# Performance work log

Measured on AMD Instinct MI355X. Metric: run time of the kernel, lower is better.

## Reference

```python
import jax, jax.numpy as jnp
import numpy as np

B, S, D = 8, 2048, 512  # batch, seq_len, lstm_hidden_dim


def setup_inputs() -> dict:
    key = jax.random.key(0)
    kq, kk, kv = jax.random.split(key, 3)
    return {
        "query": jax.random.normal(kq, (B, S, D), dtype=jnp.float32),
        "key": jax.random.normal(kk, (B, S, D), dtype=jnp.float32),
        "value": jax.random.normal(kv, (B, S, D), dtype=jnp.float32),
    }


def reference(query, key, value):
    hidden_dim = query.shape[-1]
    scale = 1.0 / jnp.sqrt(jnp.asarray(hidden_dim, dtype=jnp.float32))
    # scores: [B, S, S]
    scores = jnp.einsum("bqd,bkd->bqk", query, key) * scale
    attention_weights = jax.nn.softmax(scores, axis=-1)
    context = jnp.einsum("bqk,bkd->bqd", attention_weights, value)
    return (context, attention_weights)
```

## Files before the change

kernel.cpp:

```cpp
#include <hip/hip_runtime.h>


constexpr int BATCH = 8;
constexpr int SEQ = 2048;
constexpr int DIM = 512;
constexpr size_t QK_ELEMS = (size_t)BATCH * SEQ * DIM;

typedef __attribute__((ext_vector_type(8))) short bh8;
typedef __attribute__((ext_vector_type(4))) float f4acc;

__device__ __forceinline__ short f2bf(float f) {
  union { float f; unsigned u; } v;
  v.f = f;
  unsigned r = (v.u + 0x7FFFu + ((v.u >> 16) & 1u)) >> 16;
  return (short)r;
}

__device__ __forceinline__ void glds16(const unsigned short* g,
                                       unsigned short* l) {
  __builtin_amdgcn_global_load_lds(
      (const __attribute__((address_space(1))) unsigned int*)g,
      (__attribute__((address_space(3))) unsigned int*)l, 16, 0, 0);
}

__global__ __launch_bounds__(256) void convert_qk_kernel(
    const float* __restrict__ Q, const float* __restrict__ K,
    unsigned short* __restrict__ Qbf, unsigned short* __restrict__ Kbf) {
  const size_t i = ((size_t)blockIdx.x * 256 + threadIdx.x) * 8;
  const float sc = blockIdx.y ? 1.0f : 0.044194173824159216f;
  const float* src = blockIdx.y ? K : Q;
  unsigned short* dst = blockIdx.y ? Kbf : Qbf;
  float4 a = *(const float4*)(src + i);
  float4 b = *(const float4*)(src + i + 4);
  bh8 o;
  o[0] = f2bf(a.x * sc); o[1] = f2bf(a.y * sc);
  o[2] = f2bf(a.z * sc); o[3] = f2bf(a.w * sc);
  o[4] = f2bf(b.x * sc); o[5] = f2bf(b.y * sc);
  o[6] = f2bf(b.z * sc); o[7] = f2bf(b.w * sc);
  *(bh8*)(dst + i) = o;
}

__global__ __launch_bounds__(256) void transpose_v_kernel(
    const float* __restrict__ V, unsigned short* __restrict__ Vt) {
  __shared__ float tile[32][33];
  const int s0 = blockIdx.x * 32, d0 = blockIdx.y * 32, b = blockIdx.z;
  const float* Vb = V + (size_t)b * SEQ * DIM;
  unsigned short* Vtb = Vt + (size_t)b * DIM * SEQ;
  const int tx = threadIdx.x & 31, ty = threadIdx.x >> 5;
  for (int r = 0; r < 32; r += 8)
    tile[ty + r][tx] = Vb[(size_t)(s0 + ty + r) * DIM + (d0 + tx)];
  __syncthreads();
  for (int r = 0; r < 32; r += 8)
    Vtb[(size_t)(d0 + ty + r) * SEQ + (s0 + tx)] =
        (unsigned short)f2bf(tile[tx][ty + r]);
}

template <int KDIM, int NSTRIDE>
__device__ __forceinline__ void gemm_nt_body(
    const unsigned short* __restrict__ Arows,
    const unsigned short* __restrict__ Brows,
    float* __restrict__ Cout,
    unsigned short* As, unsigned short* Bs) {
  const int tid = threadIdx.x, lane = tid & 63, wave = tid >> 6;
  const int wm = (wave & 1) * 64, wn = (wave >> 1) * 64;
  const int srow = wave * 32 + (lane >> 2);
  const int scol = (lane & 3) * 8;
  const unsigned short* Ag = Arows + (size_t)srow * KDIM + scol;
  const unsigned short* Bg = Brows + (size_t)srow * KDIM + scol;
  unsigned short* Al = As + srow * 32 + scol;
  unsigned short* Bl = Bs + srow * 32 + scol;
  f4acc acc[4][4] = {};
  const int fr = lane & 15, fk = (lane >> 4) * 8;
  for (int k0 = 0; k0 < KDIM; k0 += 32) {
    glds16(Ag + k0, Al);
    glds16(Ag + k0 + (size_t)16 * KDIM, Al + 16 * 32);
    glds16(Bg + k0, Bl);
    glds16(Bg + k0 + (size_t)16 * KDIM, Bl + 16 * 32);
    __syncthreads();
    bh8 af[4], bf[4];
    for (int i = 0; i < 4; ++i) af[i] = *(const bh8*)(As + (wm + i * 16 + fr) * 32 + fk);
    for (int i = 0; i < 4; ++i) bf[i] = *(const bh8*)(Bs + (wn + i * 16 + fr) * 32 + fk);
    for (int mi = 0; mi < 4; ++mi)
      for (int ni = 0; ni < 4; ++ni)
        acc[mi][ni] = __builtin_amdgcn_mfma_f32_16x16x32_bf16(
            af[mi], bf[ni], acc[mi][ni], 0, 0, 0);
    __syncthreads();
  }
  const int cc = lane & 15, rr = (lane >> 4) * 4;
  for (int mi = 0; mi < 4; ++mi)
    for (int ni = 0; ni < 4; ++ni)
      for (int r = 0; r < 4; ++r)
        Cout[(size_t)(wm + mi * 16 + rr + r) * NSTRIDE + (wn + ni * 16 + cc)] =
            acc[mi][ni][r];
}

__global__ __launch_bounds__(256) void scores_kernel(
    const unsigned short* __restrict__ Qbf, const unsigned short* __restrict__ Kbf,
    float* __restrict__ W) {
  __shared__ unsigned short As[128 * 32];
  __shared__ unsigned short Bs[128 * 32];
  const int bm = blockIdx.x, bn = blockIdx.y, b = blockIdx.z;
  gemm_nt_body<DIM, SEQ>(
      Qbf + ((size_t)b * SEQ + bm * 128) * DIM,
      Kbf + ((size_t)b * SEQ + bn * 128) * DIM,
      W + (size_t)b * SEQ * SEQ + (size_t)(bm * 128) * SEQ + bn * 128, As, Bs);
}

__global__ __launch_bounds__(256) void context_kernel(
    const unsigned short* __restrict__ Wbf, const unsigned short* __restrict__ Vt,
    float* __restrict__ C) {
  __shared__ unsigned short As[128 * 32];
  __shared__ unsigned short Bs[128 * 32];
  const int bm = blockIdx.x, bn = blockIdx.y, b = blockIdx.z;
  gemm_nt_body<SEQ, DIM>(
      Wbf + ((size_t)b * SEQ + bm * 128) * SEQ,
      Vt + ((size_t)b * DIM + bn * 128) * SEQ,
      C + (size_t)b * SEQ * DIM + (size_t)(bm * 128) * DIM + bn * 128, As, Bs);
}

__global__ __launch_bounds__(256) void softmax_kernel(
    float* __restrict__ W, unsigned short* __restrict__ Wbf) {
  float* Wr = W + (size_t)blockIdx.x * SEQ;
  unsigned short* Wbr = Wbf + (size_t)blockIdx.x * SEQ;
  const int tid = threadIdx.x, lane = tid & 63, wave = tid >> 6;
  float4 a = ((const float4*)Wr)[tid];
  float4 c = ((const float4*)Wr)[tid + 256];
  float m = fmaxf(fmaxf(fmaxf(a.x, a.y), fmaxf(a.z, a.w)),
                  fmaxf(fmaxf(c.x, c.y), fmaxf(c.z, c.w)));
  for (int off = 32; off > 0; off >>= 1) m = fmaxf(m, __shfl_xor(m, off));
  __shared__ float redm[4];
  if (lane == 0) redm[wave] = m;
  __syncthreads();
  m = fmaxf(fmaxf(redm[0], redm[1]), fmaxf(redm[2], redm[3]));
  a.x = __expf(a.x - m); a.y = __expf(a.y - m);
  a.z = __expf(a.z - m); a.w = __expf(a.w - m);
  c.x = __expf(c.x - m); c.y = __expf(c.y - m);
  c.z = __expf(c.z - m); c.w = __expf(c.w - m);
  float s = (a.x + a.y + a.z + a.w) + (c.x + c.y + c.z + c.w);
  for (int off = 32; off > 0; off >>= 1) s += __shfl_xor(s, off);
  __shared__ float reds[4];
  if (lane == 0) reds[wave] = s;
  __syncthreads();
  s = reds[0] + reds[1] + reds[2] + reds[3];
  const float inv = 1.0f / s;
  a.x *= inv; a.y *= inv; a.z *= inv; a.w *= inv;
  c.x *= inv; c.y *= inv; c.z *= inv; c.w *= inv;
  ((float4*)Wr)[tid] = a;
  ((float4*)Wr)[tid + 256] = c;
  short4 ba = {f2bf(a.x), f2bf(a.y), f2bf(a.z), f2bf(a.w)};
  short4 bc = {f2bf(c.x), f2bf(c.y), f2bf(c.z), f2bf(c.w)};
  ((short4*)Wbr)[tid] = ba;
  ((short4*)Wbr)[tid + 256] = bc;
}

extern "C" void kernel_launch(void* const* d_in, const int* in_sizes, int n_in,
                              void* d_out, int out_size, void* d_ws,
                              size_t ws_size, hipStream_t stream) {
  const float* Q = (const float*)d_in[0];
  const float* K = (const float*)d_in[1];
  const float* V = (const float*)d_in[2];
  float* C = (float*)d_out;
  float* W = (float*)d_out + QK_ELEMS;
  unsigned short* Qbf = (unsigned short*)d_ws;
  unsigned short* Kbf = Qbf + QK_ELEMS;
  unsigned short* Vt  = Kbf + QK_ELEMS;
  unsigned short* Wbf = Vt + QK_ELEMS;

  convert_qk_kernel<<<dim3((unsigned)(QK_ELEMS / 8 / 256), 2), 256, 0, stream>>>(
      Q, K, Qbf, Kbf);
  transpose_v_kernel<<<dim3(SEQ / 32, DIM / 32, BATCH), 256, 0, stream>>>(V, Vt);
  scores_kernel<<<dim3(SEQ / 128, SEQ / 128, BATCH), 256, 0, stream>>>(Qbf, Kbf, W);
  softmax_kernel<<<dim3(BATCH * SEQ), 256, 0, stream>>>(W, Wbf);
  context_kernel<<<dim3(SEQ / 128, DIM / 128, BATCH), 256, 0, stream>>>(Wbf, Vt, C);
}
```

Baseline: 385.6 us.

## Store scores as bf16 via LDS staging and widen GEMM k-step to 64

The scores GEMM now writes bf16 scores into a separate workspace buffer, staged through LDS for coalesced 16-byte stores, instead of fp32 straight into the output. Softmax reads that bf16 buffer, cutting the fp32 score write and read traffic. The GEMM loop loads two 32-wide K slices per barrier pair, halving the number of syncs. Rounding scores to bf16 before softmax adds error to the attention weights, and the new buffer needs more workspace.

```diff
diff --git a/kernel.cpp b/kernel.cpp
--- a/kernel.cpp
+++ b/kernel.cpp
@@ -5,8 +5,10 @@
 constexpr int SEQ = 2048;
 constexpr int DIM = 512;
 constexpr size_t QK_ELEMS = (size_t)BATCH * SEQ * DIM;
+constexpr size_t SS_ELEMS = (size_t)BATCH * SEQ * SEQ;
 
 typedef __attribute__((ext_vector_type(8))) short bh8;
+typedef __attribute__((ext_vector_type(8))) unsigned short u16x8;
 typedef __attribute__((ext_vector_type(4))) float f4acc;
 
 __device__ __forceinline__ short f2bf(float f) {
@@ -14,6 +16,12 @@
   v.f = f;
   unsigned r = (v.u + 0x7FFFu + ((v.u >> 16) & 1u)) >> 16;
   return (short)r;
+}
+
+__device__ __forceinline__ float bf2f(unsigned short h) {
+  union { unsigned u; float f; } v;
+  v.u = (unsigned)h << 16;
+  return v.f;
 }
 
 __device__ __forceinline__ void glds16(const unsigned short* g,
@@ -55,102 +63,130 @@
         (unsigned short)f2bf(tile[tx][ty + r]);
 }
 
-template <int KDIM, int NSTRIDE>
-__device__ __forceinline__ void gemm_nt_body(
-    const unsigned short* __restrict__ Arows,
-    const unsigned short* __restrict__ Brows,
-    float* __restrict__ Cout,
-    unsigned short* As, unsigned short* Bs) {
+template <int KDIM>
+__device__ __forceinline__ void gemm_loop_nt(
+    const unsigned short* __restrict__ A, const unsigned short* __restrict__ B,
+    unsigned short* sm, f4acc acc[4][4]) {
   const int tid = threadIdx.x, lane = tid & 63, wave = tid >> 6;
   const int wm = (wave & 1) * 64, wn = (wave >> 1) * 64;
-  const int srow = wave * 32 + (lane >> 2);
-  const int scol = (lane & 3) * 8;
-  const unsigned short* Ag = Arows + (size_t)srow * KDIM + scol;
-  const unsigned short* Bg = Brows + (size_t)srow * KDIM + scol;
-  unsigned short* Al = As + srow * 32 + scol;
-  unsigned short* Bl = Bs + srow * 32 + scol;
-  f4acc acc[4][4] = {};
+  const int srow = wave * 32 + (lane >> 2), scol = (lane & 3) * 8;
+  const unsigned short* Ag = A + (size_t)srow * KDIM + scol;
+  const unsigned short* Bg = B + (size_t)srow * KDIM + scol;
+  unsigned short* As0 = sm;
+  unsigned short* As1 = sm + 4096;
+  unsigned short* Bs0 = sm + 8192;
+  unsigned short* Bs1 = sm + 12288;
+  unsigned short* Al0 = As0 + srow * 32 + scol;
+  unsigned short* Al1 = As1 + srow * 32 + scol;
+  unsigned short* Bl0 = Bs0 + srow * 32 + scol;
+  unsigned short* Bl1 = Bs1 + srow * 32 + scol;
   const int fr = lane & 15, fk = (lane >> 4) * 8;
-  for (int k0 = 0; k0 < KDIM; k0 += 32) {
-    glds16(Ag + k0, Al);
-    glds16(Ag + k0 + (size_t)16 * KDIM, Al + 16 * 32);
-    glds16(Bg + k0, Bl);
-    glds16(Bg + k0 + (size_t)16 * KDIM, Bl + 16 * 32);
+#pragma unroll 2
+  for (int k0 = 0; k0 < KDIM; k0 += 64) {
+    glds16(Ag + k0,                        Al0);
+    glds16(Ag + k0 + (size_t)16 * KDIM,    Al0 + 512);
+    glds16(Ag + k0 + 32,                   Al1);
+    glds16(Ag + k0 + 32 + (size_t)16 * KDIM, Al1 + 512);
+    glds16(Bg + k0,                        Bl0);
+    glds16(Bg + k0 + (size_t)16 * KDIM,    Bl0 + 512);
+    glds16(Bg + k0 + 32,                   Bl1);
+    glds16(Bg + k0 + 32 + (size_t)16 * KDIM, Bl1 + 512);
     __syncthreads();
-    bh8 af[4], bf[4];
-    for (int i = 0; i < 4; ++i) af[i] = *(const bh8*)(As + (wm + i * 16 + fr) * 32 + fk);
-    for (int i = 0; i < 4; ++i) bf[i] = *(const bh8*)(Bs + (wn + i * 16 + fr) * 32 + fk);
+    bh8 a0[4], a1[4], b0[4], b1[4];
+    for (int i = 0; i < 4; ++i) {
+      a0[i] = *(const bh8*)(As0 + (wm + i * 16 + fr) * 32 + fk);
+      a1[i] = *(const bh8*)(As1 + (wm + i * 16 + fr) * 32 + fk);
+      b0[i] = *(const bh8*)(Bs0 + (wn + i * 16 + fr) * 32 + fk);
+      b1[i] = *(const bh8*)(Bs1 + (wn + i * 16 + fr) * 32 + fk);
+    }
     for (int mi = 0; mi < 4; ++mi)
       for (int ni = 0; ni < 4; ++ni)
         acc[mi][ni] = __builtin_amdgcn_mfma_f32_16x16x32_bf16(
-            af[mi], bf[ni], acc[mi][ni], 0, 0, 0);
+            a0[mi], b0[ni], acc[mi][ni], 0, 0, 0);
+    for (int mi = 0; mi < 4; ++mi)
+      for (int ni = 0; ni < 4; ++ni)
+        acc[mi][ni] = __builtin_amdgcn_mfma_f32_16x16x32_bf16(
+            a1[mi], b1[ni], acc[mi][ni], 0, 0, 0);
     __syncthreads();
   }
+}
+
+__global__ __launch_bounds__(256) void scores_kernel(
+    const unsigned short* __restrict__ Qbf,
+    const unsigned short* __restrict__ Kbf,
+    unsigned short* __restrict__ Sbf) {
+  __shared__ unsigned short sm[16384];
+  const int bm = blockIdx.x, bn = blockIdx.y, b = blockIdx.z;
+  const int tid = threadIdx.x, lane = tid & 63, wave = tid >> 6;
+  const int wm = (wave & 1) * 64, wn = (wave >> 1) * 64;
+  f4acc acc[4][4] = {};
+  gemm_loop_nt<DIM>(Qbf + ((size_t)b * SEQ + bm * 128) * DIM,
+                    Kbf + ((size_t)b * SEQ + bn * 128) * DIM, sm, acc);
   const int cc = lane & 15, rr = (lane >> 4) * 4;
   for (int mi = 0; mi < 4; ++mi)
     for (int ni = 0; ni < 4; ++ni)
       for (int r = 0; r < 4; ++r)
-        Cout[(size_t)(wm + mi * 16 + rr + r) * NSTRIDE + (wn + ni * 16 + cc)] =
+        sm[(wm + mi * 16 + rr + r) * 128 + (wn + ni * 16 + cc)] =
+            (unsigned short)f2bf(acc[mi][ni][r]);
+  __syncthreads();
+  unsigned short* Sg =
+      Sbf + (size_t)b * SEQ * SEQ + (size_t)(bm * 128) * SEQ + bn * 128;
+  for (int i = 0; i < 8; ++i) {
+    int idx = i * 256 + tid;
+    int row = idx >> 4, g = (idx & 15) * 8;
+    *(u16x8*)(Sg + (size_t)row * SEQ + g) = *(const u16x8*)(sm + row * 128 + g);
+  }
+}
+
+__global__ __launch_bounds__(256) void context_kernel(
+    const unsigned short* __restrict__ Wbf,
+    const unsigned short* __restrict__ Vt, float* __restrict__ C) {
+  __shared__ unsigned short sm[16384];
+  const int bm = blockIdx.x, bn = blockIdx.y, b = blockIdx.z;
+  const int tid = threadIdx.x, lane = tid & 63, wave = tid >> 6;
+  const int wm = (wave & 1) * 64, wn = (wave >> 1) * 64;
+  f4acc acc[4][4] = {};
+  gemm_loop_nt<SEQ>(Wbf + ((size_t)b * SEQ + bm * 128) * SEQ,
+                    Vt + ((size_t)b * DIM + bn * 128) * SEQ, sm, acc);
+  float* Cb = C + (size_t)b * SEQ * DIM + (size_t)(bm * 128) * DIM + bn * 128;
+  const int cc = lane & 15, rr = (lane >> 4) * 4;
+  for (int mi = 0; mi < 4; ++mi)
+    for (int ni = 0; ni < 4; ++ni)
+      for (int r = 0; r < 4; ++r)
+        Cb[(size_t)(wm + mi * 16 + rr + r) * DIM + (wn + ni * 16 + cc)] =
             acc[mi][ni][r];
 }
 
-__global__ __launch_bounds__(256) void scores_kernel(
-    const unsigned short* __restrict__ Qbf, const unsigned short* __restrict__ Kbf,
-    float* __restrict__ W) {
-  __shared__ unsigned short As[128 * 32];
-  __shared__ unsigned short Bs[128 * 32];
-  const int bm = blockIdx.x, bn = blockIdx.y, b = blockIdx.z;
-  gemm_nt_body<DIM, SEQ>(
-      Qbf + ((size_t)b * SEQ + bm * 128) * DIM,
-      Kbf + ((size_t)b * SEQ + bn * 128) * DIM,
-      W + (size_t)b * SEQ * SEQ + (size_t)(bm * 128) * SEQ + bn * 128, As, Bs);
-}
-
-__global__ __launch_bounds__(256) void context_kernel(
-    const unsigned short* __restrict__ Wbf, const unsigned short* __restrict__ Vt,
-    float* __restrict__ C) {
-  __shared__ unsigned short As[128 * 32];
-  __shared__ unsigned short Bs[128 * 32];
-  const int bm = blockIdx.x, bn = blockIdx.y, b = blockIdx.z;
-  gemm_nt_body<SEQ, DIM>(
-      Wbf + ((size_t)b * SEQ + bm * 128) * SEQ,
-      Vt + ((size_t)b * DIM + bn * 128) * SEQ,
-      C + (size_t)b * SEQ * DIM + (size_t)(bm * 128) * DIM + bn * 128, As, Bs);
-}
-
 __global__ __launch_bounds__(256) void softmax_kernel(
-    float* __restrict__ W, unsigned short* __restrict__ Wbf) {
-  float* Wr = W + (size_t)blockIdx.x * SEQ;
-  unsigned short* Wbr = Wbf + (size_t)blockIdx.x * SEQ;
-  const int tid = threadIdx.x, lane = tid & 63, wave = tid >> 6;
-  float4 a = ((const float4*)Wr)[tid];
-  float4 c = ((const float4*)Wr)[tid + 256];
-  float m = fmaxf(fmaxf(fmaxf(a.x, a.y), fmaxf(a.z, a.w)),
-                  fmaxf(fmaxf(c.x, c.y), fmaxf(c.z, c.w)));
+    const unsigned short* __restrict__ Sbf, float* __restrict__ W,
+    unsigned short* __restrict__ Wbf) {
+  const size_t row = blockIdx.x;
+  const int tid = threadIdx.x, lane = tid & 63, wave = tid >> 6;
+  u16x8 v = *(const u16x8*)(Sbf + row * SEQ + tid * 8);
+  float x[8];
+  for (int j = 0; j < 8; ++j) x[j] = bf2f(v[j]);
+  float m = x[0];
+  for (int j = 1; j < 8; ++j) m = fmaxf(m, x[j]);
   for (int off = 32; off > 0; off >>= 1) m = fmaxf(m, __shfl_xor(m, off));
-  __shared__ float redm[4];
+  __shared__ float redm[4], reds[4];
   if (lane == 0) redm[wave] = m;
   __syncthreads();
   m = fmaxf(fmaxf(redm[0], redm[1]), fmaxf(redm[2], redm[3]));
-  a.x = __expf(a.x - m); a.y = __expf(a.y - m);
-  a.z = __expf(a.z - m); a.w = __expf(a.w - m);
-  c.x = __expf(c.x - m); c.y = __expf(c.y - m);
-  c.z = __expf(c.z - m); c.w = __expf(c.w - m);
-  float s = (a.x + a.y + a.z + a.w) + (c.x + c.y + c.z + c.w);
+  float s = 0.f;
+  for (int j = 0; j < 8; ++j) { x[j] = __expf(x[j] - m); s += x[j]; }
   for (int off = 32; off > 0; off >>= 1) s += __shfl_xor(s, off);
-  __shared__ float reds[4];
   if (lane == 0) reds[wave] = s;
   __syncthreads();
   s = reds[0] + reds[1] + reds[2] + reds[3];
   const float inv = 1.0f / s;
-  a.x *= inv; a.y *= inv; a.z *= inv; a.w *= inv;
-  c.x *= inv; c.y *= inv; c.z *= inv; c.w *= inv;
-  ((float4*)Wr)[tid] = a;
-  ((float4*)Wr)[tid + 256] = c;
-  short4 ba = {f2bf(a.x), f2bf(a.y), f2bf(a.z), f2bf(a.w)};
-  short4 bc = {f2bf(c.x), f2bf(c.y), f2bf(c.z), f2bf(c.w)};
-  ((short4*)Wbr)[tid] = ba;
-  ((short4*)Wbr)[tid + 256] = bc;
+  for (int j = 0; j < 8; ++j) x[j] *= inv;
+  float4 o0 = {x[0], x[1], x[2], x[3]}, o1 = {x[4], x[5], x[6], x[7]};
+  float* Wr = W + row * SEQ + tid * 8;
+  *(float4*)Wr = o0;
+  *(float4*)(Wr + 4) = o1;
+  u16x8 ob;
+  for (int j = 0; j < 8; ++j) ob[j] = (unsigned short)f2bf(x[j]);
+  *(u16x8*)(Wbf + row * SEQ + tid * 8) = ob;
 }
 
 extern "C" void kernel_launch(void* const* d_in, const int* in_sizes, int n_in,
@@ -164,12 +200,13 @@
   unsigned short* Qbf = (unsigned short*)d_ws;
   unsigned short* Kbf = Qbf + QK_ELEMS;
   unsigned short* Vt  = Kbf + QK_ELEMS;
-  unsigned short* Wbf = Vt + QK_ELEMS;
+  unsigned short* Sbf = Vt + QK_ELEMS;
+  unsigned short* Wbf = Sbf + SS_ELEMS;
 
   convert_qk_kernel<<<dim3((unsigned)(QK_ELEMS / 8 / 256), 2), 256, 0, stream>>>(
       Q, K, Qbf, Kbf);
   transpose_v_kernel<<<dim3(SEQ / 32, DIM / 32, BATCH), 256, 0, stream>>>(V, Vt);
-  scores_kernel<<<dim3(SEQ / 128, SEQ / 128, BATCH), 256, 0, stream>>>(Qbf, Kbf, W);
-  softmax_kernel<<<dim3(BATCH * SEQ), 256, 0, stream>>>(W, Wbf);
+  scores_kernel<<<dim3(SEQ / 128, SEQ / 128, BATCH), 256, 0, stream>>>(Qbf, Kbf, Sbf);
+  softmax_kernel<<<dim3(BATCH * SEQ), 256, 0, stream>>>(Sbf, W, Wbf);
   context_kernel<<<dim3(SEQ / 128, DIM / 128, BATCH), 256, 0, stream>>>(Wbf, Vt, C);
 }
```

Measured after the change: 377.0 us. 1.02x faster.
